# Optimization experiments

Hardware: AMD Instinct MI355X
Metric: run time of the kernel (lower is better)

Reference implementation:

```python
import jax, jax.numpy as jnp
import numpy as np
import math

B, D, NH, NS, NT = 16, 256, 512, 8, 32
NV = NS * NT          # 256 prediction variables
L, H, A = 4, 8, 64    # attention layers, heads, head dim
HA = H * A            # 512
M = 512               # mlp_dim
R = 128               # resolution
EPS = 1e-5


def setup_inputs() -> dict:
    key = jax.random.key(0)
    ks = jax.random.split(key, 32)
    s = 0.02
    inp = {
        'hist_encoded': jax.random.normal(ks[0], (B, NH, D), jnp.float32),
        'hist_true_u': jax.random.uniform(ks[1], (B, NH), jnp.float32),
        'pred_encoded': jax.random.normal(ks[2], (B, NV, D), jnp.float32),
        'pred_true_u': jax.random.uniform(ks[3], (B, NV), jnp.float32),
        # dimension shifting layer
        'ds_w': jax.random.normal(ks[4], (D, HA), jnp.float32) * s,
        'ds_b': jnp.zeros((HA,), jnp.float32),
        # per-layer, per-head key/value creators: Linear(D+1 -> A)
        'key_w': jax.random.normal(ks[5], (L, H, D + 1, A), jnp.float32) * s,
        'key_b': jnp.zeros((L, H, A), jnp.float32),
        'val_w': jax.random.normal(ks[6], (L, H, D + 1, A), jnp.float32) * s,
        'val_b': jnp.zeros((L, H, A), jnp.float32),
        # layer norms
        'ln1_g': jnp.ones((L, HA), jnp.float32),
        'ln1_b': jnp.zeros((L, HA), jnp.float32),
        'ln2_g': jnp.ones((L, HA), jnp.float32),
        'ln2_b': jnp.zeros((L, HA), jnp.float32),
        # feed-forward (mlp_layers=2): HA->M, M->M, M->HA
        'ff_w1': jax.random.normal(ks[7], (L, HA, M), jnp.float32) * s,
        'ff_b1': jnp.zeros((L, M), jnp.float32),
        'ff_w2': jax.random.normal(ks[8], (L, M, M), jnp.float32) * s,
        'ff_b2': jnp.zeros((L, M), jnp.float32),
        'ff_w3': jax.random.normal(ks[9], (L, M, HA), jnp.float32) * s,
        'ff_b3': jnp.zeros((L, HA), jnp.float32),
        # dist extractor
        'de_w': jax.random.normal(ks[10], (HA, R), jnp.float32) * s,
        'de_b': jnp.zeros((R,), jnp.float32),
        'num_series': NS,
        'num_timesteps': NT,
    }
    return inp


def _ln(x, g, b):
    m = x.mean(-1, keepdims=True)
    v = ((x - m) ** 2).mean(-1, keepdims=True)
    return g * (x - m) / jnp.sqrt(v + EPS) + b


def _forward(hist_encoded, hist_true_u, pred_encoded, pred_true_u,
             ds_w, ds_b, key_w, key_b, val_w, val_b,
             ln1_g, ln1_b, ln2_g, ln2_b,
             ff_w1, ff_b1, ff_w2, ff_b2, ff_w3, ff_b3,
             de_w, de_b):
    Bm, NVm, Dm = pred_encoded.shape
    NHm = hist_encoded.shape[1]
    Lm, Hm, _, Am = key_w.shape
    W = NHm + NVm
    # identity permutation in the source loss() -> no-op
    att = pred_encoded @ ds_w + ds_b  # [B, NV, HA]
    # key/value inputs: [hist||u ; pred||u] -> [B, W, D+1]
    ki = jnp.concatenate([
        jnp.concatenate([hist_encoded, hist_true_u[:, :, None]], axis=2),
        jnp.concatenate([pred_encoded, pred_true_u[:, :, None]], axis=2)], axis=1)
    keys = jnp.einsum('bwd,lhda->lbhwa', ki, key_w) + key_b[:, None, :, None, :]
    vals = jnp.einsum('bwd,lhda->lbhwa', ki, val_w) + val_b[:, None, :, None, :]
    # flipped-triangular mask: position w is masked iff w >= NH + v
    mask = jnp.arange(W)[None, :] >= (NHm + jnp.arange(NVm)[:, None])  # [NV, W]
    scale = Am ** (-0.5)
    for l in range(Lm):
        avh = att.reshape(Bm, NVm, Hm, Am)
        prod = jnp.einsum('bvhi,bhwi->bhvw', avh, keys[l])  # [B,H,NV,W]
        prod = jnp.where(mask, -jnp.inf, prod) * scale
        w = jax.nn.softmax(prod, axis=-1)
        a = jnp.einsum('bhvw,bhwj->bvhj', w, vals[l]).reshape(Bm, NVm, Hm * Am)
        att = _ln(att + a, ln1_g[l], ln1_b[l])
        ff = jnp.maximum(att @ ff_w1[l] + ff_b1[l], 0.0)
        ff = jnp.maximum(ff @ ff_w2[l] + ff_b2[l], 0.0)
        ff = ff @ ff_w3[l] + ff_b3[l]
        att = _ln(att + ff, ln2_g[l], ln2_b[l])
    res = de_w.shape[-1]
    target = jnp.clip(jnp.floor(pred_true_u[:, 1:] * res).astype(jnp.int32), 0, res - 1)
    logits = (att @ de_w + de_b)[:, 1:, :]
    lp = math.log(res) + jax.nn.log_softmax(logits, axis=2)
    lp = jnp.take_along_axis(lp, target[:, :, None], axis=2)[:, :, 0]
    return -lp.sum(axis=1)  # [B]


def reference(hist_encoded, hist_true_u, pred_encoded, pred_true_u,
              ds_w, ds_b, key_w, key_b, val_w, val_b,
              ln1_g, ln1_b, ln2_g, ln2_b,
              ff_w1, ff_b1, ff_w2, ff_b2, ff_w3, ff_b3,
              de_w, de_b, num_series, num_timesteps):
    assert pred_encoded.shape[1] == num_series * num_timesteps
    return _forward(hist_encoded, hist_true_u, pred_encoded, pred_true_u,
                    ds_w, ds_b, key_w, key_b, val_w, val_b,
                    ln1_g, ln1_b, ln2_g, ln2_b,
                    ff_w1, ff_b1, ff_w2, ff_b2, ff_w3, ff_b3,
                    de_w, de_b)
```

## Files before the change

### kernel.cpp

```cpp
#include <hip/hip_runtime.h>

constexpr int kB = 16, kD = 256, kNH = 512, kNV = 256, kW = 768;
constexpr int kL = 4, kH = 8, kA = 64, kHA = 512, kM = 512, kR = 128;
constexpr int kKP = 288;
constexpr int kRows = kB * kNV;

typedef __bf16 bf16x8 __attribute__((ext_vector_type(8)));
typedef __bf16 bf16x4 __attribute__((ext_vector_type(4)));
typedef float f32x4 __attribute__((ext_vector_type(4)));

__device__ inline void load_lds16(const __bf16* g, __bf16* l) {
  __builtin_amdgcn_global_load_lds(
      (const __attribute__((address_space(1))) void*)g,
      (__attribute__((address_space(3))) void*)l, 16, 0, 0);
}

constexpr int kP1 = kB * kW * kKP;
constexpr int kP2 = 4096 * kKP;
constexpr int kP3 = 12 * 512 * 512;
constexpr int kP4 = 200704;
constexpr int kP5 = 16;
constexpr int kPT = kP1 + kP2 + kP3 + kP4 + kP5;

__global__ void prep_kernel(const float* __restrict__ hist,
                            const float* __restrict__ hist_u,
                            const float* __restrict__ pred,
                            const float* __restrict__ pred_u,
                            const float* __restrict__ kw,
                            const float* __restrict__ vw,
                            const float* __restrict__ w1,
                            const float* __restrict__ w2,
                            const float* __restrict__ w3,
                            const float* __restrict__ ds_w,
                            const float* __restrict__ de_w,
                            const float* __restrict__ key_b,
                            const float* __restrict__ val_b,
                            __bf16* __restrict__ ki,
                            __bf16* __restrict__ kvwt,
                            __bf16* __restrict__ ffwt,
                            __bf16* __restrict__ ds_wt,
                            __bf16* __restrict__ de_wt,
                            float* __restrict__ kvb,
                            float* __restrict__ outz) {
  int i = blockIdx.x * 256 + threadIdx.x;
  if (i < kP1) {
    int d = i % kKP;
    int bw = i / kKP;
    int w = bw % kW;
    int b = bw / kW;
    float v = 0.f;
    if (d < 257) {
      if (w < kNH)
        v = (d < kD) ? hist[((size_t)b * kNH + w) * kD + d] : hist_u[b * kNH + w];
      else {
        int p = w - kNH;
        v = (d < kD) ? pred[((size_t)b * kNV + p) * kD + d] : pred_u[b * kNV + p];
      }
    }
    ki[i] = (__bf16)v;
  } else if (i < kP1 + kP2) {
    int j = i - kP1;
    int d = j % kKP;
    int c = j / kKP;
    float v = 0.f;
    if (d < 257) {
      bool isv = c >= 2048;
      int cc = isv ? c - 2048 : c;
      int l = cc >> 9, rest = cc & 511;
      int h = rest >> 6, a = rest & 63;
      size_t src = (((size_t)l * kH + h) * 257 + d) * kA + a;
      v = isv ? vw[src] : kw[src];
    }
    kvwt[j] = (__bf16)v;
  } else if (i < kP1 + kP2 + kP3) {
    int j = i - kP1 - kP2;
    int k = j & 511;
    int n = (j >> 9) & 511;
    int mat = j >> 18;
    int l = mat / 3, which = mat % 3;
    const float* src = which == 0 ? w1 : which == 1 ? w2 : w3;
    ffwt[j] = (__bf16)src[((size_t)l * 512 + k) * 512 + n];
  } else if (i < kP1 + kP2 + kP3 + kP4) {
    int j = i - kP1 - kP2 - kP3;
    if (j < 131072) {
      int n = j >> 8, k = j & 255;
      ds_wt[j] = (__bf16)ds_w[k * 512 + n];
    } else if (j < 196608) {
      int jj = j - 131072;
      int n = jj >> 9, k = jj & 511;
      de_wt[jj] = (__bf16)de_w[k * 128 + n];
    } else {
      int c = j - 196608;
      bool isv = c >= 2048;
      int cc = isv ? c - 2048 : c;
      int l = cc >> 9, rest = cc & 511;
      kvb[c] = isv ? val_b[l * 512 + rest] : key_b[l * 512 + rest];
    }
  } else if (i < kPT) {
    outz[i - kP1 - kP2 - kP3 - kP4] = 0.f;
  }
}

template <int BN, int OMODE, bool RELU, bool KIMAP, bool BIASROW, int DEPTH>
__device__ __forceinline__ void gemm_core(
    int bxv, int byv, const __bf16* __restrict__ A,
    const __bf16* __restrict__ Bt, const float* __restrict__ bias,
    void* __restrict__ Cout, __bf16* __restrict__ Cout2, int K, int lda,
    int ldc, __bf16* Sm) {
  constexpr int JN = BN / 32;
  constexpr int BROWS = BN / 4;
  constexpr int SSTEP = (128 + BN) * 32;
  constexpr int LPS = (BN == 128) ? 4 : 3;
  constexpr int AH = DEPTH - 1;
  const int t = threadIdx.x;
  const int wid = t >> 6;
  const int lane = t & 63;
  const int bm = byv * 128;
  const int bn = bxv * BN;
  const int wm = (wid >> 1) * 64;
  const int wn = (wid & 1) * (BN / 2);
  const int sr = lane >> 2, sc = lane & 3;
  const int skey = (sr >> 1) & 3;
  const int abase = KIMAP ? ((bm >> 8) * 768 + 512 + (bm & 255)) : bm;
  const __bf16* Ag = A + (size_t)(abase + wid * 32 + sr) * lda + (sc ^ skey) * 8;
  const __bf16* Bg = Bt + (size_t)(bn + wid * BROWS + sr) * K + (sc ^ skey) * 8;

  auto stage = [&](int k0, __bf16* buf) {
    __bf16* As = buf;
    __bf16* Bs = buf + 4096;
    load_lds16(Ag + k0, As + (wid * 32) * 32);
    load_lds16(Ag + (size_t)16 * lda + k0, As + (wid * 32 + 16) * 32);
    load_lds16(Bg + k0, Bs + (wid * BROWS) * 32);
    if (BN == 128)
      load_lds16(Bg + (size_t)16 * K + k0, Bs + (wid * BROWS + 16) * 32);
  };

  f32x4 acc[4][JN] = {};
  const int q = lane >> 4, mr = lane & 15;
  const int rkey = (mr >> 1) & 3;
  const int nst = K >> 5;
  __bf16* b0 = Sm;
  __bf16* b1 = Sm + SSTEP;
  __bf16* b2 = Sm + 2 * SSTEP;
  __bf16* b3 = (DEPTH == 4) ? Sm + 3 * SSTEP : nullptr;
  stage(0, b0);
  stage(32, b1);
  if constexpr (DEPTH == 4) stage(64, b2);
  asm volatile("s_waitcnt vmcnt(%0)" ::"n"((AH - 1) * LPS) : "memory");
  __builtin_amdgcn_s_barrier();
  for (int k = 0; k < nst; ++k) {
    if (k + AH < nst) {
      if constexpr (DEPTH == 4) stage((k + AH) << 5, b3);
      else stage((k + AH) << 5, b2);
    }
    bf16x8 af[4], bfr[JN];
#pragma unroll
    for (int i = 0; i < 4; ++i)
      af[i] = *(const bf16x8*)(b0 + (wm + i * 16 + mr) * 32 + (q ^ rkey) * 8);
#pragma unroll
    for (int j = 0; j < JN; ++j)
      bfr[j] =
          *(const bf16x8*)(b0 + 4096 + (wn + j * 16 + mr) * 32 + (q ^ rkey) * 8);
#pragma unroll
    for (int i = 0; i < 4; ++i)
#pragma unroll
      for (int j = 0; j < JN; ++j)
        acc[i][j] = __builtin_amdgcn_mfma_f32_16x16x32_bf16(af[i], bfr[j],
                                                            acc[i][j], 0, 0, 0);
    if (k + AH + 1 <= nst)
      asm volatile("s_waitcnt vmcnt(%0)" ::"n"((AH - 1) * LPS) : "memory");
    else if (DEPTH == 4 && k + AH == nst + 1)
      asm volatile("s_waitcnt vmcnt(%0)" ::"n"(LPS) : "memory");
    else
      asm volatile("s_waitcnt vmcnt(0)" ::: "memory");
    __builtin_amdgcn_s_barrier();
    if constexpr (DEPTH == 4) {
      __bf16* tp = b0; b0 = b1; b1 = b2; b2 = b3; b3 = tp;
    } else {
      __bf16* tp = b0; b0 = b1; b1 = b2; b2 = tp;
    }
  }
  if (OMODE == 1) {
    constexpr int PS = BN + 8;
    __bf16* Cs = Sm;
#pragma unroll
    for (int j = 0; j < JN; ++j) {
      float bscol = BIASROW ? 0.f : bias[bn + wn + j * 16 + mr];
#pragma unroll
      for (int i = 0; i < 4; ++i) {
#pragma unroll
        for (int r = 0; r < 4; ++r) {
          float v = acc[i][j][r] +
                    (BIASROW ? bias[bm + wm + i * 16 + q * 4 + r] : bscol);
          if (RELU) v = fmaxf(v, 0.f);
          Cs[(wm + i * 16 + q * 4 + r) * PS + wn + j * 16 + mr] = (__bf16)v;
        }
      }
    }
    __syncthreads();
    constexpr int lpr = BN / 8;
    constexpr int rpi = 512 / BN;
    const int rl = lane / lpr, cl = (lane % lpr) * 8;
#pragma unroll
    for (int it = 0; it < BN / 16; ++it) {
      int row = wid * 32 + it * rpi + rl;
      bf16x8 v = *(const bf16x8*)&Cs[row * PS + cl];
      *(bf16x8*)((__bf16*)Cout + (size_t)(bm + row) * ldc + bn + cl) = v;
    }
  } else {
    constexpr int PSF = BN + 4;
    float* Csf = (float*)Sm;
#pragma unroll
    for (int j = 0; j < JN; ++j) {
      float bscol = bias[bn + wn + j * 16 + mr];
#pragma unroll
      for (int i = 0; i < 4; ++i) {
#pragma unroll
        for (int r = 0; r < 4; ++r) {
          float v = acc[i][j][r] + bscol;
          if (RELU) v = fmaxf(v, 0.f);
          Csf[(wm + i * 16 + q * 4 + r) * PSF + wn + j * 16 + mr] = v;
        }
      }
    }
    __syncthreads();
    const int rl = lane >> 4, cl = (lane & 15) * 4;
#pragma unroll
    for (int it = 0; it < 8; ++it) {
      int row = wid * 32 + it * 4 + rl;
      f32x4 v = *(const f32x4*)&Csf[row * PSF + cl];
      size_t gidx = (size_t)(bm + row) * ldc + bn + cl;
      *(f32x4*)((float*)Cout + gidx) = v;
      bf16x4 vb = {(__bf16)v[0], (__bf16)v[1], (__bf16)v[2], (__bf16)v[3]};
      *(bf16x4*)(Cout2 + gidx) = vb;
    }
  }
}

__global__ __launch_bounds__(256) void gemm3_kernel(
    const __bf16* __restrict__ ki, const __bf16* __restrict__ ds_wt,
    const float* __restrict__ ds_b, float* __restrict__ att,
    __bf16* __restrict__ att_bf, const __bf16* __restrict__ kv_wt,
    const float* __restrict__ kvb, __bf16* __restrict__ kvs_k,
    __bf16* __restrict__ vT) {
  __shared__ __bf16 smem[24576];
  int bid = blockIdx.x;
  if (bid < 256) {
    gemm_core<64, 2, false, true, false, 3>(bid & 7, bid >> 3, ki, ds_wt, ds_b,
                                            att, att_bf, 256, kKP, 512, smem);
  } else if (bid < 1792) {
    int b2 = bid - 256;
    gemm_core<128, 1, false, false, false, 3>(b2 & 15, b2 >> 4, ki, kv_wt, kvb,
                                              kvs_k, nullptr, kKP, kKP, 2048,
                                              smem);
  } else {
    int b3 = bid - 1792;
    gemm_core<128, 1, false, false, true, 3>(b3 % 96, b3 / 96,
                                             kv_wt + (size_t)2048 * kKP, ki,
                                             kvb + 2048, vT, nullptr, kKP, kKP,
                                             12288, smem);
  }
}

template <bool RELU>
__global__ __launch_bounds__(256) void gemm_ff_kernel(
    const __bf16* __restrict__ A, const __bf16* __restrict__ Bt,
    const float* __restrict__ bias, __bf16* __restrict__ Cout) {
  __shared__ __bf16 smem[24576];
  gemm_core<64, 1, RELU, false, false, 4>(blockIdx.x, blockIdx.y, A, Bt, bias,
                                          Cout, nullptr, 512, 512, 512, smem);
}

__global__ __launch_bounds__(256) void attn_mfma_kernel(
    const __bf16* __restrict__ attbf, const __bf16* __restrict__ kvs_k,
    const __bf16* __restrict__ vT, __bf16* __restrict__ outbf, int l) {
  const int id = blockIdx.x;
  const int kk = id >> 3;
  const int b = ((kk >> 5) << 3) | (id & 7);
  const int qt = kk & 3;
  const int h = (kk >> 2) & 7;
  __shared__ __bf16 Ks[64 * 72];
  __shared__ __bf16 Vt[64 * 72];
  __shared__ __bf16 Ps[64 * 72];
  const int t = threadIdx.x;
  const int w = t >> 6, lane = t & 63;
  const int quad = lane >> 4, mr = lane & 15;
  bf16x8 aq[2];
  {
    const __bf16* qp = attbf + ((size_t)(b * kNV + qt * 64 + w * 16 + mr) * kHA +
                                h * kA + quad * 8);
    aq[0] = *(const bf16x8*)qp;
    aq[1] = *(const bf16x8*)(qp + 32);
  }
  f32x4 o[4] = {};
  float m_ = -1e30f, l_ = 0.f;
  const int cmax = kNH + qt * 64;
  const int pr = t >> 2, pc = t & 3;
  const __bf16* kbase = kvs_k + ((size_t)(b * kW + pr) * 2048 + l * 512 + h * kA);
  const __bf16* vbase = vT + (size_t)(l * 512 + h * kA + pr) * 12288 + b * kW;
  bf16x8 kc0, kc1, vc0, vc1;
  kc0 = *(const bf16x8*)(kbase + pc * 8);
  kc1 = *(const bf16x8*)(kbase + pc * 8 + 32);
  vc0 = *(const bf16x8*)(vbase + pc * 16);
  vc1 = *(const bf16x8*)(vbase + pc * 16 + 8);
  for (int c0 = 0; c0 <= cmax; c0 += 64) {
    __syncthreads();
    *(bf16x8*)&Ks[pr * 72 + pc * 8] = kc0;
    *(bf16x8*)&Ks[pr * 72 + pc * 8 + 32] = kc1;
    *(bf16x8*)&Vt[pr * 72 + pc * 16] = vc0;
    *(bf16x8*)&Vt[pr * 72 + pc * 16 + 8] = vc1;
    __syncthreads();
    if (c0 + 64 <= cmax) {
      const __bf16* kp = kbase + (size_t)(c0 + 64) * 2048;
      const __bf16* vp = vbase + c0 + 64;
      kc0 = *(const bf16x8*)(kp + pc * 8);
      kc1 = *(const bf16x8*)(kp + pc * 8 + 32);
      vc0 = *(const bf16x8*)(vp + pc * 16);
      vc1 = *(const bf16x8*)(vp + pc * 16 + 8);
    }
    f32x4 s[4];
#pragma unroll
    for (int j = 0; j < 4; ++j) {
      bf16x8 ak0 = *(const bf16x8*)&Ks[(j * 16 + mr) * 72 + quad * 8];
      bf16x8 ak1 = *(const bf16x8*)&Ks[(j * 16 + mr) * 72 + quad * 8 + 32];
      f32x4 z = {};
      z = __builtin_amdgcn_mfma_f32_16x16x32_bf16(ak0, aq[0], z, 0, 0, 0);
      z = __builtin_amdgcn_mfma_f32_16x16x32_bf16(ak1, aq[1], z, 0, 0, 0);
      s[j] = z;
    }
    const int lim = cmax - c0;
    float sv[16], mx = -1e30f;
#pragma unroll
    for (int j = 0; j < 4; ++j)
#pragma unroll
      for (int r = 0; r < 4; ++r) {
        int p = j * 16 + quad * 4 + r;
        float x = (p < lim + mr) ? s[j][r] * 0.125f : -1e30f;
        sv[j * 4 + r] = x;
        mx = fmaxf(mx, x);
      }
    mx = fmaxf(mx, __shfl_xor(mx, 16));
    mx = fmaxf(mx, __shfl_xor(mx, 32));
    float mnew = fmaxf(m_, mx);
    float corr = __expf(m_ - mnew);
    float rs = 0.f;
#pragma unroll
    for (int i = 0; i < 16; ++i) {
      sv[i] = __expf(sv[i] - mnew);
      rs += sv[i];
    }
    rs += __shfl_xor(rs, 16);
    rs += __shfl_xor(rs, 32);
    l_ = l_ * corr + rs;
    m_ = mnew;
#pragma unroll
    for (int j = 0; j < 4; ++j) {
      bf16x4 pk = {(__bf16)sv[j * 4 + 0], (__bf16)sv[j * 4 + 1],
                   (__bf16)sv[j * 4 + 2], (__bf16)sv[j * 4 + 3]};
      *(bf16x4*)&Ps[(w * 16 + mr) * 72 + j * 16 + quad * 4] = pk;
    }
#pragma unroll
    for (int r = 0; r < 4; ++r) {
      float cr = __shfl(corr, quad * 4 + r);
#pragma unroll
      for (int j = 0; j < 4; ++j) o[j][r] *= cr;
    }
    bf16x8 ap0 = *(const bf16x8*)&Ps[(w * 16 + mr) * 72 + quad * 8];
    bf16x8 ap1 = *(const bf16x8*)&Ps[(w * 16 + mr) * 72 + quad * 8 + 32];
#pragma unroll
    for (int j = 0; j < 4; ++j) {
      bf16x8 b0 = *(const bf16x8*)&Vt[(j * 16 + mr) * 72 + quad * 8];
      bf16x8 b1 = *(const bf16x8*)&Vt[(j * 16 + mr) * 72 + quad * 8 + 32];
      o[j] = __builtin_amdgcn_mfma_f32_16x16x32_bf16(ap0, b0, o[j], 0, 0, 0);
      o[j] = __builtin_amdgcn_mfma_f32_16x16x32_bf16(ap1, b1, o[j], 0, 0, 0);
    }
  }
  float invl = 1.f / l_;
#pragma unroll
  for (int r = 0; r < 4; ++r) {
    float ir = __shfl(invl, quad * 4 + r);
    int row = b * kNV + qt * 64 + w * 16 + quad * 4 + r;
#pragma unroll
    for (int j = 0; j < 4; ++j)
      outbf[(size_t)row * kHA + h * kA + j * 16 + mr] = (__bf16)(o[j][r] * ir);
  }
}

__global__ __launch_bounds__(256) void add_ln_kernel(
    float* __restrict__ att, const __bf16* __restrict__ addbf,
    const float* __restrict__ g, const float* __restrict__ be,
    __bf16* __restrict__ attbf) {
  const int w = threadIdx.x >> 6, lane = threadIdx.x & 63;
  const int row = blockIdx.x * 4 + w;
  const int c0 = lane * 8;
  const size_t base = (size_t)row * kHA + c0;
  float4 a0 = *(const float4*)(att + base);
  float4 a1 = *(const float4*)(att + base + 4);
  bf16x8 dv = *(const bf16x8*)(addbf + base);
  float x[8] = {a0.x + (float)dv[0], a0.y + (float)dv[1], a0.z + (float)dv[2],
                a0.w + (float)dv[3], a1.x + (float)dv[4], a1.y + (float)dv[5],
                a1.z + (float)dv[6], a1.w + (float)dv[7]};
  float s = 0.f, q = 0.f;
#pragma unroll
  for (int j = 0; j < 8; ++j) { s += x[j]; q += x[j] * x[j]; }
#pragma unroll
  for (int o = 1; o < 64; o <<= 1) {
    s += __shfl_xor(s, o);
    q += __shfl_xor(q, o);
  }
  const float mean = s * (1.f / kHA);
  const float inv = rsqrtf(q * (1.f / kHA) - mean * mean + 1e-5f);
  float4 g0 = *(const float4*)(g + c0);
  float4 g1 = *(const float4*)(g + c0 + 4);
  float4 e0 = *(const float4*)(be + c0);
  float4 e1 = *(const float4*)(be + c0 + 4);
  float y[8];
  y[0] = g0.x * (x[0] - mean) * inv + e0.x;
  y[1] = g0.y * (x[1] - mean) * inv + e0.y;
  y[2] = g0.z * (x[2] - mean) * inv + e0.z;
  y[3] = g0.w * (x[3] - mean) * inv + e0.w;
  y[4] = g1.x * (x[4] - mean) * inv + e1.x;
  y[5] = g1.y * (x[5] - mean) * inv + e1.y;
  y[6] = g1.z * (x[6] - mean) * inv + e1.z;
  y[7] = g1.w * (x[7] - mean) * inv + e1.w;
  *(float4*)(att + base) = (float4){y[0], y[1], y[2], y[3]};
  *(float4*)(att + base + 4) = (float4){y[4], y[5], y[6], y[7]};
  bf16x8 yb = {(__bf16)y[0], (__bf16)y[1], (__bf16)y[2], (__bf16)y[3],
               (__bf16)y[4], (__bf16)y[5], (__bf16)y[6], (__bf16)y[7]};
  *(bf16x8*)(attbf + base) = yb;
}

__global__ __launch_bounds__(256) void de_loss_kernel(
    const __bf16* __restrict__ attbf, const __bf16* __restrict__ de_wt,
    const float* __restrict__ de_b, const float* __restrict__ pred_u,
    float* __restrict__ out) {
  const int blk = blockIdx.x;
  const int t = threadIdx.x;
  const int w = t >> 6, lane = t & 63, quad = lane >> 4, mr = lane & 15;
  const int row0 = blk * 64 + w * 16;
  f32x4 acc[8] = {};
  const __bf16* Ap = attbf + (size_t)(row0 + mr) * kHA + quad * 8;
#pragma unroll 4
  for (int k0 = 0; k0 < 512; k0 += 32) {
    bf16x8 a = *(const bf16x8*)(Ap + k0);
#pragma unroll
    for (int j = 0; j < 8; ++j) {
      bf16x8 bb =
          *(const bf16x8*)(de_wt + (size_t)(j * 16 + mr) * 512 + k0 + quad * 8);
      acc[j] = __builtin_amdgcn_mfma_f32_16x16x32_bf16(a, bb, acc[j], 0, 0, 0);
    }
  }
  float dbv[8];
#pragma unroll
  for (int j = 0; j < 8; ++j) dbv[j] = de_b[j * 16 + mr];
  float lpacc = 0.f;
#pragma unroll
  for (int r = 0; r < 4; ++r) {
    int row = row0 + quad * 4 + r;
    int v = row & 255;
    float lg[8], mx = -1e30f;
#pragma unroll
    for (int j = 0; j < 8; ++j) {
      lg[j] = acc[j][r] + dbv[j];
      mx = fmaxf(mx, lg[j]);
    }
    mx = fmaxf(mx, __shfl_xor(mx, 1));
    mx = fmaxf(mx, __shfl_xor(mx, 2));
    mx = fmaxf(mx, __shfl_xor(mx, 4));
    mx = fmaxf(mx, __shfl_xor(mx, 8));
    float se = 0.f;
#pragma unroll
    for (int j = 0; j < 8; ++j) se += __expf(lg[j] - mx);
    se += __shfl_xor(se, 1);
    se += __shfl_xor(se, 2);
    se += __shfl_xor(se, 4);
    se += __shfl_xor(se, 8);
    float lse = mx + __logf(se);
    float u = pred_u[(row >> 8) * 256 + v];
    int tgt = (int)floorf(u * 128.f);
    tgt = max(0, min(127, tgt));
    float cand = (mr == (tgt & 15)) ? lg[tgt >> 4] : 0.f;
    cand += __shfl_xor(cand, 1);
    cand += __shfl_xor(cand, 2);
    cand += __shfl_xor(cand, 4);
    cand += __shfl_xor(cand, 8);
    float lp = (v >= 1) ? (4.8520302639196171f + cand - lse) : 0.f;
    lpacc += lp;
  }
  lpacc += __shfl_xor(lpacc, 16);
  lpacc += __shfl_xor(lpacc, 32);
  __shared__ float red[4];
  if (lane == 0) red[w] = lpacc;
  __syncthreads();
  if (t == 0)
    atomicAdd(&out[blk >> 2], -(red[0] + red[1] + red[2] + red[3]));
}

extern "C" void kernel_launch(void* const* d_in, const int* in_sizes, int n_in,
                              void* d_out, int out_size, void* d_ws, size_t ws_size,
                              hipStream_t stream) {
  const float* hist   = (const float*)d_in[0];
  const float* hist_u = (const float*)d_in[1];
  const float* pred   = (const float*)d_in[2];
  const float* pred_u = (const float*)d_in[3];
  const float* ds_w   = (const float*)d_in[4];
  const float* ds_b   = (const float*)d_in[5];
  const float* key_w  = (const float*)d_in[6];
  const float* key_b  = (const float*)d_in[7];
  const float* val_w  = (const float*)d_in[8];
  const float* val_b  = (const float*)d_in[9];
  const float* ln1_g  = (const float*)d_in[10];
  const float* ln1_b  = (const float*)d_in[11];
  const float* ln2_g  = (const float*)d_in[12];
  const float* ln2_b  = (const float*)d_in[13];
  const float* ff_w1  = (const float*)d_in[14];
  const float* ff_b1  = (const float*)d_in[15];
  const float* ff_w2  = (const float*)d_in[16];
  const float* ff_b2  = (const float*)d_in[17];
  const float* ff_w3  = (const float*)d_in[18];
  const float* ff_b3  = (const float*)d_in[19];
  const float* de_w   = (const float*)d_in[20];
  const float* de_b   = (const float*)d_in[21];
  float* out = (float*)d_out;

  char* ws = (char*)d_ws;
  size_t off = 0;
  auto alloc = [&](size_t bytes) { char* p = ws + off; off += bytes; return p; };
  __bf16* ki_bf  = (__bf16*)alloc((size_t)kB * kW * kKP * 2);
  __bf16* kv_wt  = (__bf16*)alloc((size_t)4096 * kKP * 2);
  __bf16* ffw_t  = (__bf16*)alloc((size_t)12 * 512 * 512 * 2);
  __bf16* ds_wt  = (__bf16*)alloc((size_t)512 * 256 * 2);
  __bf16* de_wt  = (__bf16*)alloc((size_t)128 * 512 * 2);
  float*  kvb    = (float*)alloc((size_t)4096 * 4);
  __bf16* kvs_k  = (__bf16*)alloc((size_t)kB * kW * 2048 * 2);
  __bf16* vT     = (__bf16*)alloc((size_t)2048 * 12288 * 2);
  float*  att    = (float*)alloc((size_t)kRows * kHA * 4);
  __bf16* att_bf = (__bf16*)alloc((size_t)kRows * kHA * 2);
  __bf16* tmp_bf = (__bf16*)alloc((size_t)kRows * kHA * 2);
  __bf16* ff1_bf = (__bf16*)alloc((size_t)kRows * kM * 2);
  __bf16* ff2_bf = (__bf16*)alloc((size_t)kRows * kM * 2);

  prep_kernel<<<(kPT + 255) / 256, 256, 0, stream>>>(
      hist, hist_u, pred, pred_u, key_w, val_w, ff_w1, ff_w2, ff_w3, ds_w, de_w,
      key_b, val_b, ki_bf, kv_wt, ffw_t, ds_wt, de_wt, kvb, out);

  gemm3_kernel<<<3328, 256, 0, stream>>>(ki_bf, ds_wt, ds_b, att, att_bf, kv_wt,
                                         kvb, kvs_k, vT);

  for (int l = 0; l < kL; ++l) {
    attn_mfma_kernel<<<512, 256, 0, stream>>>(att_bf, kvs_k, vT, tmp_bf, l);
    add_ln_kernel<<<kRows / 4, 256, 0, stream>>>(att, tmp_bf, ln1_g + l * kHA,
                                                 ln1_b + l * kHA, att_bf);
    gemm_ff_kernel<true><<<dim3(kM / 64, kRows / 128), 256, 0, stream>>>(
        att_bf, ffw_t + (size_t)(l * 3) * 262144, ff_b1 + l * kM, ff1_bf);
    gemm_ff_kernel<true><<<dim3(kM / 64, kRows / 128), 256, 0, stream>>>(
        ff1_bf, ffw_t + (size_t)(l * 3 + 1) * 262144, ff_b2 + l * kM, ff2_bf);
    gemm_ff_kernel<false><<<dim3(kHA / 64, kRows / 128), 256, 0, stream>>>(
        ff2_bf, ffw_t + (size_t)(l * 3 + 2) * 262144, ff_b3 + l * kHA, tmp_bf);
    add_ln_kernel<<<kRows / 4, 256, 0, stream>>>(att, tmp_bf, ln2_g + l * kHA,
                                                 ln2_b + l * kHA, att_bf);
  }
  de_loss_kernel<<<64, 256, 0, stream>>>(att_bf, de_wt, de_b, pred_u, out);
}
```

Baseline: 436.3 us.

## Tile weight transposes through LDS and fuse final layernorm into loss kernel

The prep kernel's weight transposes (key/value, feed-forward, ds, de) now stage 32-wide tiles through padded shared memory, so global reads and writes are both coalesced instead of strided per element. Separately, the last layer's residual-add plus layernorm moves into the de_loss kernel, which normalizes 64 rows into swizzled LDS and reads the GEMM A operand from there. This drops one kernel launch and an activation write plus re-read. The cost is a serial layernorm prologue in a 64-block loss kernel and more complex prep indexing.

```diff
diff --git a/kernel.cpp b/kernel.cpp
--- a/kernel.cpp
+++ b/kernel.cpp
@@ -16,11 +16,7 @@
 }
 
 constexpr int kP1 = kB * kW * kKP;
-constexpr int kP2 = 4096 * kKP;
-constexpr int kP3 = 12 * 512 * 512;
-constexpr int kP4 = 200704;
-constexpr int kP5 = 16;
-constexpr int kPT = kP1 + kP2 + kP3 + kP4 + kP5;
+constexpr int kPrepBlocks = 17681;
 
 __global__ void prep_kernel(const float* __restrict__ hist,
                             const float* __restrict__ hist_u,
@@ -42,8 +38,11 @@
                             __bf16* __restrict__ de_wt,
                             float* __restrict__ kvb,
                             float* __restrict__ outz) {
-  int i = blockIdx.x * 256 + threadIdx.x;
-  if (i < kP1) {
+  __shared__ float ld[2080];
+  const int bid = blockIdx.x;
+  const int t = threadIdx.x;
+  if (bid < 13824) {
+    int i = bid * 256 + t;
     int d = i % kKP;
     int bw = i / kKP;
     int w = bw % kW;
@@ -58,46 +57,81 @@
       }
     }
     ki[i] = (__bf16)v;
-  } else if (i < kP1 + kP2) {
-    int j = i - kP1;
-    int d = j % kKP;
-    int c = j / kKP;
-    float v = 0.f;
-    if (d < 257) {
-      bool isv = c >= 2048;
-      int cc = isv ? c - 2048 : c;
+  } else if (bid < 14400) {
+    int bb = bid - 13824;
+    bool isv = bb >= 288;
+    int rem = isv ? bb - 288 : bb;
+    int pair = rem / 9;
+    int dt = rem - pair * 9;
+    int d0 = dt * 32;
+    const float* src = (isv ? vw : kw) + (size_t)pair * 257 * 64;
+    int a = t & 63, dg = t >> 6;
+#pragma unroll
+    for (int ii = 0; ii < 8; ++ii) {
+      int d = d0 + dg * 8 + ii;
+      ld[(dg * 8 + ii) * 65 + a] = (d < 257) ? src[(size_t)d * 64 + a] : 0.f;
+    }
+    __syncthreads();
+    int r = t >> 2, seg = t & 3;
+    bf16x8 v;
+#pragma unroll
+    for (int j = 0; j < 8; ++j) v[j] = (__bf16)ld[(seg * 8 + j) * 65 + r];
+    *(bf16x8*)&kvwt[((size_t)(isv ? 2048 : 0) + pair * 64 + r) * 288 + d0 +
+                    seg * 8] = v;
+  } else if (bid < 17472) {
+    int cc = bid - 14400;
+    int mat = cc >> 8;
+    int tile = cc & 255;
+    int n0 = (tile & 15) * 32, k0 = (tile >> 4) * 32;
+    int l = mat / 3, which = mat - l * 3;
+    const float* src = (which == 0 ? w1 : which == 1 ? w2 : w3) +
+                       (size_t)l * 262144;
+    int col = t & 31, kr = t >> 5;
+#pragma unroll
+    for (int p = 0; p < 4; ++p)
+      ld[(kr + p * 8) * 33 + col] = src[(size_t)(k0 + kr + p * 8) * 512 + n0 + col];
+    __syncthreads();
+    int nr = t >> 3, seg = t & 7;
+    bf16x4 v;
+#pragma unroll
+    for (int j = 0; j < 4; ++j) v[j] = (__bf16)ld[(seg * 4 + j) * 33 + nr];
+    *(bf16x4*)&ffwt[(size_t)mat * 262144 + (n0 + nr) * 512 + k0 + seg * 4] = v;
+  } else if (bid < 17600) {
+    int cc = bid - 17472;
+    int n0 = (cc & 15) * 32, k0 = (cc >> 4) * 32;
+    int col = t & 31, kr = t >> 5;
+#pragma unroll
+    for (int p = 0; p < 4; ++p)
+      ld[(kr + p * 8) * 33 + col] = ds_w[(size_t)(k0 + kr + p * 8) * 512 + n0 + col];
+    __syncthreads();
+    int nr = t >> 3, seg = t & 7;
+    bf16x4 v;
+#pragma unroll
+    for (int j = 0; j < 4; ++j) v[j] = (__bf16)ld[(seg * 4 + j) * 33 + nr];
+    *(bf16x4*)&ds_wt[(n0 + nr) * 256 + k0 + seg * 4] = v;
+  } else if (bid < 17664) {
+    int cc = bid - 17600;
+    int n0 = (cc & 3) * 32, k0 = (cc >> 2) * 32;
+    int col = t & 31, kr = t >> 5;
+#pragma unroll
+    for (int p = 0; p < 4; ++p)
+      ld[(kr + p * 8) * 33 + col] = de_w[(size_t)(k0 + kr + p * 8) * 128 + n0 + col];
+    __syncthreads();
+    int nr = t >> 3, seg = t & 7;
+    bf16x4 v;
+#pragma unroll
+    for (int j = 0; j < 4; ++j) v[j] = (__bf16)ld[(seg * 4 + j) * 33 + nr];
+    *(bf16x4*)&de_wt[(n0 + nr) * 512 + k0 + seg * 4] = v;
+  } else {
+    int j = (bid - 17664) * 256 + t;
+    if (j < 4096) {
+      bool isv = j >= 2048;
+      int cc = isv ? j - 2048 : j;
       int l = cc >> 9, rest = cc & 511;
-      int h = rest >> 6, a = rest & 63;
-      size_t src = (((size_t)l * kH + h) * 257 + d) * kA + a;
-      v = isv ? vw[src] : kw[src];
-    }
-    kvwt[j] = (__bf16)v;
-  } else if (i < kP1 + kP2 + kP3) {
-    int j = i - kP1 - kP2;
-    int k = j & 511;
-    int n = (j >> 9) & 511;
-    int mat = j >> 18;
-    int l = mat / 3, which = mat % 3;
-    const float* src = which == 0 ? w1 : which == 1 ? w2 : w3;
-    ffwt[j] = (__bf16)src[((size_t)l * 512 + k) * 512 + n];
-  } else if (i < kP1 + kP2 + kP3 + kP4) {
-    int j = i - kP1 - kP2 - kP3;
-    if (j < 131072) {
-      int n = j >> 8, k = j & 255;
-      ds_wt[j] = (__bf16)ds_w[k * 512 + n];
-    } else if (j < 196608) {
-      int jj = j - 131072;
-      int n = jj >> 9, k = jj & 511;
-      de_wt[jj] = (__bf16)de_w[k * 128 + n];
-    } else {
-      int c = j - 196608;
-      bool isv = c >= 2048;
-      int cc = isv ? c - 2048 : c;
-      int l = cc >> 9, rest = cc & 511;
-      kvb[c] = isv ? val_b[l * 512 + rest] : key_b[l * 512 + rest];
-    }
-  } else if (i < kPT) {
-    outz[i - kP1 - kP2 - kP3 - kP4] = 0.f;
+      kvb[j] = isv ? val_b[l * 512 + rest] : key_b[l * 512 + rest];
+    } else if (j < 4112) {
+      outz[j - 4096] = 0.f;
+    }
   }
 }
 
@@ -431,18 +465,60 @@
 }
 
 __global__ __launch_bounds__(256) void de_loss_kernel(
-    const __bf16* __restrict__ attbf, const __bf16* __restrict__ de_wt,
-    const float* __restrict__ de_b, const float* __restrict__ pred_u,
-    float* __restrict__ out) {
+    const float* __restrict__ att, const __bf16* __restrict__ fbf,
+    const float* __restrict__ g2, const float* __restrict__ b2,
+    const __bf16* __restrict__ de_wt, const float* __restrict__ de_b,
+    const float* __restrict__ pred_u, float* __restrict__ out) {
+  __shared__ __bf16 Als[64 * 512];
+  __shared__ float red[4];
   const int blk = blockIdx.x;
   const int t = threadIdx.x;
   const int w = t >> 6, lane = t & 63, quad = lane >> 4, mr = lane & 15;
+  {
+    const int c0 = lane * 8;
+    float4 ga = *(const float4*)(g2 + c0);
+    float4 gb = *(const float4*)(g2 + c0 + 4);
+    float4 ba = *(const float4*)(b2 + c0);
+    float4 bb = *(const float4*)(b2 + c0 + 4);
+    for (int rr = 0; rr < 16; ++rr) {
+      const int lrow = w * 16 + rr;
+      const size_t base = (size_t)(blk * 64 + lrow) * 512 + c0;
+      float4 a0 = *(const float4*)(att + base);
+      float4 a1 = *(const float4*)(att + base + 4);
+      bf16x8 dv = *(const bf16x8*)(fbf + base);
+      float x[8] = {a0.x + (float)dv[0], a0.y + (float)dv[1],
+                    a0.z + (float)dv[2], a0.w + (float)dv[3],
+                    a1.x + (float)dv[4], a1.y + (float)dv[5],
+                    a1.z + (float)dv[6], a1.w + (float)dv[7]};
+      float s = 0.f, q = 0.f;
+#pragma unroll
+      for (int j = 0; j < 8; ++j) { s += x[j]; q += x[j] * x[j]; }
+#pragma unroll
+      for (int o = 1; o < 64; o <<= 1) {
+        s += __shfl_xor(s, o);
+        q += __shfl_xor(q, o);
+      }
+      const float mean = s * (1.f / kHA);
+      const float inv = rsqrtf(q * (1.f / kHA) - mean * mean + 1e-5f);
+      bf16x8 yv = {(__bf16)(ga.x * (x[0] - mean) * inv + ba.x),
+                   (__bf16)(ga.y * (x[1] - mean) * inv + ba.y),
+                   (__bf16)(ga.z * (x[2] - mean) * inv + ba.z),
+                   (__bf16)(ga.w * (x[3] - mean) * inv + ba.w),
+                   (__bf16)(gb.x * (x[4] - mean) * inv + bb.x),
+                   (__bf16)(gb.y * (x[5] - mean) * inv + bb.y),
+                   (__bf16)(gb.z * (x[6] - mean) * inv + bb.z),
+                   (__bf16)(gb.w * (x[7] - mean) * inv + bb.w)};
+      *(bf16x8*)&Als[lrow * 512 + ((lane ^ (lrow & 7)) << 3)] = yv;
+    }
+  }
+  __syncthreads();
   const int row0 = blk * 64 + w * 16;
+  const int lrowA = w * 16 + mr;
   f32x4 acc[8] = {};
-  const __bf16* Ap = attbf + (size_t)(row0 + mr) * kHA + quad * 8;
 #pragma unroll 4
   for (int k0 = 0; k0 < 512; k0 += 32) {
-    bf16x8 a = *(const bf16x8*)(Ap + k0);
+    const int grp = (((k0 >> 3) + quad) ^ (lrowA & 7)) << 3;
+    bf16x8 a = *(const bf16x8*)&Als[lrowA * 512 + grp];
 #pragma unroll
     for (int j = 0; j < 8; ++j) {
       bf16x8 bb =
@@ -489,7 +565,6 @@
   }
   lpacc += __shfl_xor(lpacc, 16);
   lpacc += __shfl_xor(lpacc, 32);
-  __shared__ float red[4];
   if (lane == 0) red[w] = lpacc;
   __syncthreads();
   if (t == 0)
@@ -540,7 +615,7 @@
   __bf16* ff1_bf = (__bf16*)alloc((size_t)kRows * kM * 2);
   __bf16* ff2_bf = (__bf16*)alloc((size_t)kRows * kM * 2);
 
-  prep_kernel<<<(kPT + 255) / 256, 256, 0, stream>>>(
+  prep_kernel<<<kPrepBlocks, 256, 0, stream>>>(
       hist, hist_u, pred, pred_u, key_w, val_w, ff_w1, ff_w2, ff_w3, ds_w, de_w,
       key_b, val_b, ki_bf, kv_wt, ffw_t, ds_wt, de_wt, kvb, out);
 
@@ -557,8 +632,12 @@
         ff1_bf, ffw_t + (size_t)(l * 3 + 1) * 262144, ff_b2 + l * kM, ff2_bf);
     gemm_ff_kernel<false><<<dim3(kHA / 64, kRows / 128), 256, 0, stream>>>(
         ff2_bf, ffw_t + (size_t)(l * 3 + 2) * 262144, ff_b3 + l * kHA, tmp_bf);
-    add_ln_kernel<<<kRows / 4, 256, 0, stream>>>(att, tmp_bf, ln2_g + l * kHA,
-                                                 ln2_b + l * kHA, att_bf);
-  }
-  de_loss_kernel<<<64, 256, 0, stream>>>(att_bf, de_wt, de_b, pred_u, out);
-}
+    if (l < kL - 1)
+      add_ln_kernel<<<kRows / 4, 256, 0, stream>>>(att, tmp_bf,
+                                                   ln2_g + l * kHA,
+                                                   ln2_b + l * kHA, att_bf);
+  }
+  de_loss_kernel<<<64, 256, 0, stream>>>(att, tmp_bf, ln2_g + 3 * kHA,
+                                         ln2_b + 3 * kHA, de_wt, de_b, pred_u,
+                                         out);
+}
```

Result: faster. 413.3 us (-5.3%).
